# Performance work log

Hardware: AMD Instinct MI355X
Metric: run time of the kernel (lower is better)

The kernel has to match this reference:

```python
import jax, jax.numpy as jnp
import numpy as np

# dims
N, M, L, E = 50000, 1024, 3, 200000      # tgt nodes, src nodes, subtokens/node, edges
HID, EMB, VOCAB = 512, 256, 512
N_SLT, N_SRT = 4, 5                       # SLT edge types (messages), SRT edge types (output head)
W_SCALE = 0.02


def setup_inputs() -> dict:
    key = jax.random.key(0)
    ks = jax.random.split(key, 20)
    inp = {
        "tgt_x": jax.random.randint(ks[0], (N, L), 0, VOCAB),
        "x": jax.random.normal(ks[1], (M, HID), jnp.float32),
        "tgt_edge_index": jax.random.randint(ks[2], (2, E), 0, N),
        "tgt_edge_type": jax.random.randint(ks[3], (E,), 0, N_SLT),
        "embed_table": jax.random.normal(ks[4], (VOCAB, EMB), jnp.float32) * W_SCALE,
        # GCN layer 1 (called twice in the original forward) and layer 3 params
        "W_h1": jax.random.normal(ks[5], (EMB, EMB), jnp.float32) * W_SCALE,
        "W_rel1": jax.random.normal(ks[6], (N_SLT, EMB, EMB), jnp.float32) * W_SCALE,
        "W_src1": jax.random.normal(ks[7], (HID, EMB), jnp.float32) * W_SCALE,
        "W_h3": jax.random.normal(ks[8], (EMB, EMB), jnp.float32) * W_SCALE,
        "W_rel3": jax.random.normal(ks[9], (N_SLT, EMB, EMB), jnp.float32) * W_SCALE,
        "W_src3": jax.random.normal(ks[10], (HID, EMB), jnp.float32) * W_SCALE,
        # output heads
        "Wz": jax.random.normal(ks[11], (EMB, VOCAB), jnp.float32) * W_SCALE,
        "bz": jnp.zeros((VOCAB,), jnp.float32),
        "Wg": jax.random.normal(ks[12], (2 * EMB, N_SRT), jnp.float32) * W_SCALE,
        "bg": jnp.zeros((N_SRT,), jnp.float32),
    }
    return inp


def _gcn_layer(x_src, h, edge_index, edge_type, W_h, W_rel, W_src):
    """Relational GCN decoder layer with cross-attention to encoder nodes."""
    k = x_src @ W_src                                   # [M, EMB]
    attn = jax.nn.softmax(h @ k.T / jnp.sqrt(jnp.float32(EMB)), axis=1)  # [N, M]
    ctx = attn @ k                                      # [N, EMB]
    # per-edge-type transform first ([N, T, EMB]), then gather per edge
    h_t = jnp.einsum('nd,tdf->ntf', h, W_rel)           # [N, N_SLT, EMB]
    src, tgt = edge_index[0], edge_index[1]
    msg = h_t[src, edge_type]                           # [E, EMB] gather
    agg = jax.ops.segment_sum(msg, tgt, num_segments=h.shape[0])  # [N, EMB]
    return jax.nn.relu(h @ W_h + agg + ctx)


def reference(tgt_x, x, tgt_edge_index, tgt_edge_type, embed_table,
              W_h1, W_rel1, W_src1, W_h3, W_rel3, W_src3, Wz, bz, Wg, bg):
    # embedding + reduction over subtokens
    h = embed_table[tgt_x].sum(axis=1)                  # [N, EMB]
    # original code calls gcn1 twice, then gcn3 (gcn2 unused in training path)
    h = _gcn_layer(x, h, tgt_edge_index, tgt_edge_type, W_h1, W_rel1, W_src1)
    h = _gcn_layer(x, h, tgt_edge_index, tgt_edge_type, W_h1, W_rel1, W_src1)
    h = _gcn_layer(x, h, tgt_edge_index, tgt_edge_type, W_h3, W_rel3, W_src3)
    # node head
    node_pred = jax.nn.log_softmax(h @ Wz + bz, axis=1)  # [N, VOCAB]
    # edge head: gather [2,E,EMB] -> permute -> [E, 2*EMB]
    ef = h[tgt_edge_index]                               # [2, E, EMB]
    ef = jnp.transpose(ef, (1, 0, 2)).reshape(E, 2 * EMB)
    edge_pred = jax.nn.log_softmax(ef @ Wg + bg, axis=1)  # [E, N_SRT]
    return node_pred, edge_pred
```

## Files before the change

kernel.cpp:

```cpp
#include <hip/hip_runtime.h>
#include <hip/hip_bf16.h>
#include <cstdint>

#define N_NODES 50000
#define M_SRC   1024
#define E_EDGES 200000
#define EMB     256
#define HIDN    512
#define VOCABSZ 512
#define KW      1280

typedef __attribute__((ext_vector_type(8))) short bf16x8;
typedef __attribute__((ext_vector_type(4))) short bf16x4;
typedef __attribute__((ext_vector_type(4))) float f32x4;

__device__ inline short f2b(float f) {
    __hip_bfloat16 b = __float2bfloat16(f);
    return *reinterpret_cast<short*>(&b);
}
__device__ inline float b2f(short s) {
    __hip_bfloat16 b = *reinterpret_cast<__hip_bfloat16*>(&s);
    return __bfloat162float(b);
}

__device__ inline void gload16(const void* g, void* l) {
    __builtin_amdgcn_global_load_lds(
        (const __attribute__((address_space(1))) unsigned int*)g,
        (__attribute__((address_space(3))) unsigned int*)l,
        16, 0, 0);
}

__device__ inline void tr_read2(unsigned addr, bf16x4& lo, bf16x4& hi) {
    asm volatile("ds_read_b64_tr_b16 %0, %2\n\tds_read_b64_tr_b16 %1, %2 offset:512"
                 : "=&v"(lo), "=&v"(hi) : "v"(addr));
}

__global__ void embed_kernel(const int* __restrict__ tgt_x,
                             const float* __restrict__ table,
                             short* __restrict__ h)
{
    int n = blockIdx.x, d = threadIdx.x;
    const int* tx = tgt_x + (size_t)n * 3;
    float s = table[(size_t)tx[0] * EMB + d]
            + table[(size_t)tx[1] * EMB + d]
            + table[(size_t)tx[2] * EMB + d];
    h[(size_t)n * EMB + d] = f2b(s);
}

__global__ void convert_kernel(const float* __restrict__ in, short* __restrict__ out, int n)
{
    int i = blockIdx.x * 256 + threadIdx.x;
    if (i * 4 < n) {
        float4 v = *(const float4*)&in[i * 4];
        short4 o;
        o.x = f2b(v.x); o.y = f2b(v.y); o.z = f2b(v.z); o.w = f2b(v.w);
        *(short4*)&out[i * 4] = o;
    }
}

template<typename TIN>
__global__ void transpose_kernel(const TIN* __restrict__ in, short* __restrict__ out, int R, int C)
{
    __shared__ float t[32][33];
    int tx = threadIdx.x & 31, ty = threadIdx.x >> 5;
    int r0 = blockIdx.y * 32, c0 = blockIdx.x * 32;
#pragma unroll
    for (int i = 0; i < 4; i++) {
        int r = ty + i * 8;
        TIN v = in[(size_t)(r0 + r) * C + c0 + tx];
        if constexpr (sizeof(TIN) == 4) t[r][tx] = v;
        else                            t[r][tx] = b2f(v);
    }
    __syncthreads();
#pragma unroll
    for (int i = 0; i < 4; i++) {
        int r = ty + i * 8;
        out[(size_t)(c0 + r) * R + r0 + tx] = f2b(t[tx][r]);
    }
}

__global__ void transposeW_kernel(const float* __restrict__ Wh1, const float* __restrict__ Wh3,
                                  const float* __restrict__ Wr1, const float* __restrict__ Wr3,
                                  short* __restrict__ Wcat1, short* __restrict__ Wcat3)
{
    __shared__ float t[32][33];
    const int z = blockIdx.z;
    const float* in; short* outp; int coloff;
    if (z == 0)      { in = Wh1;                               outp = Wcat1; coloff = 0; }
    else if (z == 1) { in = Wh3;                               outp = Wcat3; coloff = 0; }
    else if (z < 6)  { in = Wr1 + (size_t)(z - 2) * EMB * EMB; outp = Wcat1; coloff = 256 + (z - 2) * 256; }
    else             { in = Wr3 + (size_t)(z - 6) * EMB * EMB; outp = Wcat3; coloff = 256 + (z - 6) * 256; }
    int tx = threadIdx.x & 31, ty = threadIdx.x >> 5;
    int r0 = blockIdx.y * 32, c0 = blockIdx.x * 32;
#pragma unroll
    for (int i = 0; i < 4; i++) {
        int r = ty + i * 8;
        t[r][tx] = in[(size_t)(r0 + r) * EMB + c0 + tx];
    }
    __syncthreads();
#pragma unroll
    for (int i = 0; i < 4; i++) {
        int r = ty + i * 8;
        outp[(size_t)(c0 + r) * KW + coloff + r0 + tx] = f2b(t[tx][r]);
    }
}

template<int MODE>
__global__ __launch_bounds__(256) void mgemm(
    const short* __restrict__ A, const short* __restrict__ BT,
    void* __restrict__ outp, const float* __restrict__ aux,
    const float* __restrict__ bias, int NR, int K, int J)
{
    __shared__ short As[128 * 40];
    __shared__ short Bs[128 * 40];
    const int tid  = threadIdx.x;
    const int n0   = blockIdx.x * 128;
    const int j0   = blockIdx.y * 128;
    const int lane = tid & 63, wid = tid >> 6;
    const int wr   = wid >> 1, wc = wid & 1;

    f32x4 acc[4][4];
#pragma unroll
    for (int m = 0; m < 4; m++)
#pragma unroll
        for (int n = 0; n < 4; n++) acc[m][n] = (f32x4){0.f, 0.f, 0.f, 0.f};

    for (int kt = 0; kt < K; kt += 32) {
#pragma unroll
        for (int r = 0; r < 2; r++) {
            int idx = tid + r * 256;
            int row = idx >> 2, ko = (idx & 3) * 8;
            int n = n0 + row;
            bf16x8 av = {0, 0, 0, 0, 0, 0, 0, 0};
            if (n < NR) av = *(const bf16x8*)&A[(size_t)n * K + kt + ko];
            *(bf16x8*)&As[row * 40 + ko] = av;
            *(bf16x8*)&Bs[row * 40 + ko] = *(const bf16x8*)&BT[(size_t)(j0 + row) * K + kt + ko];
        }
        __syncthreads();
        bf16x8 af[4], bfr[4];
#pragma unroll
        for (int m = 0; m < 4; m++)
            af[m] = *(const bf16x8*)&As[(wr * 64 + m * 16 + (lane & 15)) * 40 + (lane >> 4) * 8];
#pragma unroll
        for (int n = 0; n < 4; n++)
            bfr[n] = *(const bf16x8*)&Bs[(wc * 64 + n * 16 + (lane & 15)) * 40 + (lane >> 4) * 8];
#pragma unroll
        for (int m = 0; m < 4; m++)
#pragma unroll
            for (int n = 0; n < 4; n++)
                acc[m][n] = __builtin_amdgcn_mfma_f32_16x16x32_bf16(af[m], bfr[n], acc[m][n], 0, 0, 0);
        __syncthreads();
    }

#pragma unroll
    for (int m = 0; m < 4; m++) {
        int rbase = wr * 64 + m * 16 + ((lane >> 4) * 4);
#pragma unroll
        for (int r = 0; r < 4; r++) {
            int n_g = n0 + rbase + r;
            if (n_g >= NR) continue;
#pragma unroll
            for (int nn = 0; nn < 4; nn++) {
                int j_g = j0 + wc * 64 + nn * 16 + (lane & 15);
                ((short*)outp)[(size_t)n_g * J + j_g] = f2b(acc[m][nn][r]);
            }
        }
    }
}

__global__ __launch_bounds__(256) void mgemm_wide(
    const short* __restrict__ A1, const short* __restrict__ A2,
    const short* __restrict__ BT, short* __restrict__ outp,
    const float* __restrict__ aux, int NR)
{
    __shared__ short As[64 * 40];
    __shared__ short Bs[256 * 40];
    const int tid  = threadIdx.x;
    const int n0   = blockIdx.x * 64;
    const int lane = tid & 63, wid = tid >> 6;
    const int wr   = wid >> 1, wc = wid & 1;
    const int l4 = lane >> 4, l15 = lane & 15;

    f32x4 acc[2][8];
#pragma unroll
    for (int m = 0; m < 2; m++)
#pragma unroll
        for (int n = 0; n < 8; n++) acc[m][n] = (f32x4){0.f, 0.f, 0.f, 0.f};

    for (int kt = 0; kt < KW; kt += 32) {
        {
            int row = tid >> 2, ko = (tid & 3) * 8;
            int n = n0 + row;
            bf16x8 av = {0, 0, 0, 0, 0, 0, 0, 0};
            if (n < NR) {
                const short* ap = (kt < 256) ? &A1[(size_t)n * 256 + kt + ko]
                                             : &A2[(size_t)n * 1024 + (kt - 256) + ko];
                av = *(const bf16x8*)ap;
            }
            *(bf16x8*)&As[row * 40 + ko] = av;
        }
#pragma unroll
        for (int r = 0; r < 4; r++) {
            int idx = tid + r * 256;
            int row = idx >> 2, ko = (idx & 3) * 8;
            *(bf16x8*)&Bs[row * 40 + ko] = *(const bf16x8*)&BT[(size_t)row * KW + kt + ko];
        }
        __syncthreads();
        bf16x8 af[2], bfr[8];
#pragma unroll
        for (int m = 0; m < 2; m++)
            af[m] = *(const bf16x8*)&As[(wr * 32 + m * 16 + l15) * 40 + l4 * 8];
#pragma unroll
        for (int n = 0; n < 8; n++)
            bfr[n] = *(const bf16x8*)&Bs[(wc * 128 + n * 16 + l15) * 40 + l4 * 8];
#pragma unroll
        for (int m = 0; m < 2; m++)
#pragma unroll
            for (int n = 0; n < 8; n++)
                acc[m][n] = __builtin_amdgcn_mfma_f32_16x16x32_bf16(af[m], bfr[n], acc[m][n], 0, 0, 0);
        __syncthreads();
    }

#pragma unroll
    for (int m = 0; m < 2; m++) {
        int rbase = wr * 32 + m * 16 + l4 * 4;
#pragma unroll
        for (int r = 0; r < 4; r++) {
            int n_g = n0 + rbase + r;
            if (n_g >= NR) continue;
#pragma unroll
            for (int nn = 0; nn < 8; nn++) {
                int j_g = wc * 128 + nn * 16 + l15;
                float v = acc[m][nn][r] + aux[(size_t)n_g * 256 + j_g];
                outp[(size_t)n_g * 256 + j_g] = f2b(fmaxf(v, 0.f));
            }
        }
    }
}

__global__ __launch_bounds__(128, 2) void attn_flash(
    const short* __restrict__ h, const short* __restrict__ kb,
    float* __restrict__ C, int NR)
{
    __shared__ short ks[2][32 * 256];
    __shared__ short Ps[64 * 36];

    const int tid = threadIdx.x;
    const int lane = tid & 63, wv = tid >> 6;
    const int l4 = lane >> 4, l15 = lane & 15;
    const int n0 = blockIdx.x * 64;

    auto LOFF = [](int key, int d8) {
        return (d8 & 1) * 8 + (key & 3) * 16 + ((key >> 3) & 3) * 64
             + ((key >> 2) & 1) * 256 + (d8 >> 1) * 512;
    };
    int keyq[8], d8q[8];
#pragma unroll
    for (int q = 0; q < 8; q++) {
        int ci = wv * 64 + lane + q * 128;
        d8q[q]  = (ci & 1) | ((ci >> 6) << 1);
        keyq[q] = ((ci >> 1) & 3) | (((ci >> 5) & 1) << 2) | (((ci >> 3) & 3) << 3);
    }

    bf16x8 hreg[2][8];
#pragma unroll
    for (int rg = 0; rg < 2; rg++) {
        int n = n0 + wv * 32 + rg * 16 + l15;
        const short* hp = &h[(size_t)(n < NR ? n : 0) * 256 + l4 * 8];
#pragma unroll
        for (int kst = 0; kst < 8; kst++) hreg[rg][kst] = *(const bf16x8*)&hp[kst * 32];
        if (n >= NR) {
#pragma unroll
            for (int kst = 0; kst < 8; kst++) hreg[rg][kst] = (bf16x8){0, 0, 0, 0, 0, 0, 0, 0};
        }
    }

#pragma unroll
    for (int q = 0; q < 8; q++)
        gload16(&kb[(size_t)keyq[q] * 256 + d8q[q] * 8],
                (char*)&ks[0][0] + q * 2048 + wv * 1024);
    __syncthreads();

    const unsigned ksbase = (unsigned)(uintptr_t)&ks[0][0];
    const unsigned trlane = 2u * (unsigned)(l15 + l4 * 64);

    f32x4 oacc[2][16];
#pragma unroll
    for (int rg = 0; rg < 2; rg++)
#pragma unroll
        for (int mm = 0; mm < 16; mm++) oacc[rg][mm] = (f32x4){0.f, 0.f, 0.f, 0.f};
    float lsum[2] = {0.f, 0.f};

    for (int c = 0; c < 32; c++) {
        const int cur = c & 1;
        if (c + 1 < 32) {
            const short* kbn = kb + (size_t)(c + 1) * 32 * 256;
#pragma unroll
            for (int q = 0; q < 8; q++)
                gload16(&kbn[(size_t)keyq[q] * 256 + d8q[q] * 8],
                        (char*)&ks[cur ^ 1][0] + q * 2048 + wv * 1024);
        }

        f32x4 sacc[2][2];
#pragma unroll
        for (int rg = 0; rg < 2; rg++) {
            sacc[rg][0] = (f32x4){0.f, 0.f, 0.f, 0.f};
            sacc[rg][1] = (f32x4){0.f, 0.f, 0.f, 0.f};
        }
        __builtin_amdgcn_s_setprio(1);
#pragma unroll
        for (int kst = 0; kst < 8; kst++) {
#pragma unroll
            for (int m = 0; m < 2; m++) {
                int krow = m * 16 + l15;
                bf16x8 afk = *(const bf16x8*)&ks[cur][LOFF(krow, kst * 4 + l4)];
                sacc[0][m] = __builtin_amdgcn_mfma_f32_16x16x32_bf16(afk, hreg[0][kst], sacc[0][m], 0, 0, 0);
                sacc[1][m] = __builtin_amdgcn_mfma_f32_16x16x32_bf16(afk, hreg[1][kst], sacc[1][m], 0, 0, 0);
            }
        }
        __builtin_amdgcn_s_setprio(0);

#pragma unroll
        for (int rg = 0; rg < 2; rg++) {
            int prow = wv * 32 + rg * 16 + l15;
            float psum = 0.f;
#pragma unroll
            for (int m = 0; m < 2; m++) {
                float p0 = __expf(sacc[rg][m][0] * 0.0625f);
                float p1 = __expf(sacc[rg][m][1] * 0.0625f);
                float p2 = __expf(sacc[rg][m][2] * 0.0625f);
                float p3 = __expf(sacc[rg][m][3] * 0.0625f);
                psum += (p0 + p1) + (p2 + p3);
                short4 pk;
                pk.x = f2b(p0); pk.y = f2b(p1); pk.z = f2b(p2); pk.w = f2b(p3);
                *(short4*)&Ps[prow * 36 + m * 16 + l4 * 4] = pk;
            }
            psum += __shfl_xor(psum, 16);
            psum += __shfl_xor(psum, 32);
            lsum[rg] += psum;
        }

        bf16x8 bf2[2];
#pragma unroll
        for (int rg = 0; rg < 2; rg++)
            bf2[rg] = *(const bf16x8*)&Ps[(wv * 32 + rg * 16 + l15) * 36 + l4 * 8];
        unsigned trb = ksbase + (unsigned)(cur * 16384) + trlane;
#pragma unroll
        for (int g = 0; g < 2; g++) {
            bf16x4 lo[8], hi[8];
#pragma unroll
            for (int q = 0; q < 8; q++)
                tr_read2(trb + (unsigned)((g * 8 + q) * 1024), lo[q], hi[q]);
            asm volatile("s_waitcnt lgkmcnt(0)" ::: "memory");
            __builtin_amdgcn_sched_barrier(0);
            __builtin_amdgcn_s_setprio(1);
#pragma unroll
            for (int q = 0; q < 8; q++) {
                bf16x8 af2;
#pragma unroll
                for (int t2 = 0; t2 < 4; t2++) { af2[t2] = lo[q][t2]; af2[t2 + 4] = hi[q][t2]; }
                oacc[0][g * 8 + q] = __builtin_amdgcn_mfma_f32_16x16x32_bf16(af2, bf2[0], oacc[0][g * 8 + q], 0, 0, 0);
                oacc[1][g * 8 + q] = __builtin_amdgcn_mfma_f32_16x16x32_bf16(af2, bf2[1], oacc[1][g * 8 + q], 0, 0, 0);
            }
            __builtin_amdgcn_s_setprio(0);
        }

        __syncthreads();
    }

#pragma unroll
    for (int rg = 0; rg < 2; rg++) {
        float li = 1.0f / lsum[rg];
        int hr = n0 + wv * 32 + rg * 16 + l15;
        if (hr >= NR) continue;
#pragma unroll
        for (int mm = 0; mm < 16; mm++) {
            float4 v;
            v.x = oacc[rg][mm][0] * li;
            v.y = oacc[rg][mm][1] * li;
            v.z = oacc[rg][mm][2] * li;
            v.w = oacc[rg][mm][3] * li;
            *(float4*)&C[(size_t)hr * 256 + mm * 16 + l4 * 4] = v;
        }
    }
}

__global__ void hist_kernel(const int* __restrict__ ei, int* __restrict__ deg)
{
    int e = blockIdx.x * 256 + threadIdx.x;
    if (e < E_EDGES) atomicAdd(&deg[ei[E_EDGES + e]], 1);
}

__global__ void scan1_kernel(const int* __restrict__ deg, int* __restrict__ incl,
                             int* __restrict__ bsum)
{
    __shared__ int s[256];
    int i = blockIdx.x * 256 + threadIdx.x;
    int v = (i < N_NODES) ? deg[i] : 0;
    s[threadIdx.x] = v;
    __syncthreads();
#pragma unroll
    for (int off = 1; off < 256; off <<= 1) {
        int t = (threadIdx.x >= off) ? s[threadIdx.x - off] : 0;
        __syncthreads();
        s[threadIdx.x] += t;
        __syncthreads();
    }
    if (i < N_NODES) incl[i] = s[threadIdx.x];
    if (threadIdx.x == 255) bsum[blockIdx.x] = s[255];
}

__global__ void scan2_kernel(int* __restrict__ bsum, int nb)
{
    __shared__ int s[256];
    int v = (threadIdx.x < nb) ? bsum[threadIdx.x] : 0;
    s[threadIdx.x] = v;
    __syncthreads();
#pragma unroll
    for (int off = 1; off < 256; off <<= 1) {
        int t = (threadIdx.x >= off) ? s[threadIdx.x - off] : 0;
        __syncthreads();
        s[threadIdx.x] += t;
        __syncthreads();
    }
    if (threadIdx.x < nb) bsum[threadIdx.x] = s[threadIdx.x];
}

__global__ void scan3_kernel(const int* __restrict__ deg, const int* __restrict__ incl,
                             const int* __restrict__ bsum, int* __restrict__ row_ptr,
                             int* __restrict__ cursor)
{
    int i = blockIdx.x * 256 + threadIdx.x;
    if (i >= N_NODES) return;
    int pref = (blockIdx.x > 0) ? bsum[blockIdx.x - 1] : 0;
    int start = pref + incl[i] - deg[i];
    row_ptr[i] = start;
    cursor[i]  = start;
    if (i == N_NODES - 1) row_ptr[N_NODES] = pref + incl[i];
}

__global__ void fill_kernel(const int* __restrict__ ei, const int* __restrict__ et,
                            int* __restrict__ cursor, int* __restrict__ eidx)
{
    int e = blockIdx.x * 256 + threadIdx.x;
    if (e >= E_EDGES) return;
    int tg = ei[E_EDGES + e];
    int slot = atomicAdd(&cursor[tg], 1);
    eidx[slot] = ei[e] | (et[e] << 16);
}

__global__ void agg2_kernel(const int* __restrict__ row_ptr, const int* __restrict__ eidx,
                            const short* __restrict__ h, short* __restrict__ Bagg)
{
    int w = (blockIdx.x * 256 + threadIdx.x) >> 6;
    if (w >= N_NODES) return;
    int lane = threadIdx.x & 63;
    int s0 = row_ptr[w], s1 = row_ptr[w + 1];
    float a0[4] = {0, 0, 0, 0}, a1[4] = {0, 0, 0, 0}, a2[4] = {0, 0, 0, 0}, a3[4] = {0, 0, 0, 0};
    for (int i = s0; i < s1; i++) {
        int p = eidx[i];
        int s = p & 0xFFFF, t = p >> 16;
        short4 g = *(const short4*)&h[(size_t)s * EMB + lane * 4];
        float f0 = b2f(g.x), f1 = b2f(g.y), f2 = b2f(g.z), f3 = b2f(g.w);
        if (t == 0)      { a0[0] += f0; a0[1] += f1; a0[2] += f2; a0[3] += f3; }
        else if (t == 1) { a1[0] += f0; a1[1] += f1; a1[2] += f2; a1[3] += f3; }
        else if (t == 2) { a2[0] += f0; a2[1] += f1; a2[2] += f2; a2[3] += f3; }
        else             { a3[0] += f0; a3[1] += f1; a3[2] += f2; a3[3] += f3; }
    }
    short4 o;
    o.x = f2b(a0[0]); o.y = f2b(a0[1]); o.z = f2b(a0[2]); o.w = f2b(a0[3]);
    *(short4*)&Bagg[(size_t)w * 1024 + 0 * 256 + lane * 4] = o;
    o.x = f2b(a1[0]); o.y = f2b(a1[1]); o.z = f2b(a1[2]); o.w = f2b(a1[3]);
    *(short4*)&Bagg[(size_t)w * 1024 + 1 * 256 + lane * 4] = o;
    o.x = f2b(a2[0]); o.y = f2b(a2[1]); o.z = f2b(a2[2]); o.w = f2b(a2[3]);
    *(short4*)&Bagg[(size_t)w * 1024 + 2 * 256 + lane * 4] = o;
    o.x = f2b(a3[0]); o.y = f2b(a3[1]); o.z = f2b(a3[2]); o.w = f2b(a3[3]);
    *(short4*)&Bagg[(size_t)w * 1024 + 3 * 256 + lane * 4] = o;
}

__global__ __launch_bounds__(512, 2) void head_kernel(
    const short* __restrict__ hmat, const short* __restrict__ WzT,
    const float* __restrict__ bz, float* __restrict__ out, int NR)
{
    __shared__ short hs[64 * 256];
    __shared__ float redm[64 * 8];
    __shared__ float reds[64 * 8];

    const int tid = threadIdx.x;
    const int lane = tid & 63, wv = tid >> 6;
    const int l4 = lane >> 4, l15 = lane & 15;
    const int n0 = blockIdx.x * 64;

#pragma unroll
    for (int i = 0; i < 4; i++) {
        int idx = tid + i * 512;
        int row = idx >> 5, kg = idx & 31;
        bf16x8 v = {0, 0, 0, 0, 0, 0, 0, 0};
        if (n0 + row < NR) v = *(const bf16x8*)&hmat[(size_t)(n0 + row) * 256 + kg * 8];
        *(bf16x8*)&hs[(row * 256 + kg * 8) ^ ((row & 7) << 3)] = v;
    }
    __syncthreads();

    f32x4 acc[4][4];
#pragma unroll
    for (int m = 0; m < 4; m++)
#pragma unroll
        for (int n = 0; n < 4; n++) acc[m][n] = (f32x4){0.f, 0.f, 0.f, 0.f};

#pragma unroll
    for (int kt = 0; kt < 256; kt += 32) {
        bf16x8 af[4], bfr[4];
#pragma unroll
        for (int m = 0; m < 4; m++) {
            int row = m * 16 + l15;
            af[m] = *(const bf16x8*)&hs[(row * 256 + kt + l4 * 8) ^ ((row & 7) << 3)];
        }
#pragma unroll
        for (int n = 0; n < 4; n++) {
            int col = wv * 64 + n * 16 + l15;
            bfr[n] = *(const bf16x8*)&WzT[(size_t)col * 256 + kt + l4 * 8];
        }
#pragma unroll
        for (int m = 0; m < 4; m++)
#pragma unroll
            for (int n = 0; n < 4; n++)
                acc[m][n] = __builtin_amdgcn_mfma_f32_16x16x32_bf16(af[m], bfr[n], acc[m][n], 0, 0, 0);
    }

    float bcol[4];
#pragma unroll
    for (int n = 0; n < 4; n++) bcol[n] = bz[wv * 64 + n * 16 + l15];
#pragma unroll
    for (int m = 0; m < 4; m++)
#pragma unroll
        for (int n = 0; n < 4; n++)
#pragma unroll
            for (int r = 0; r < 4; r++) acc[m][n][r] += bcol[n];

    float lg[4][4];
#pragma unroll
    for (int m = 0; m < 4; m++)
#pragma unroll
        for (int r = 0; r < 4; r++) {
            float v = fmaxf(fmaxf(acc[m][0][r], acc[m][1][r]), fmaxf(acc[m][2][r], acc[m][3][r]));
            v = fmaxf(v, __shfl_xor(v, 1));
            v = fmaxf(v, __shfl_xor(v, 2));
            v = fmaxf(v, __shfl_xor(v, 4));
            v = fmaxf(v, __shfl_xor(v, 8));
            if (l15 == 0) redm[(m * 16 + l4 * 4 + r) * 8 + wv] = v;
        }
    __syncthreads();
#pragma unroll
    for (int m = 0; m < 4; m++)
#pragma unroll
        for (int r = 0; r < 4; r++) {
            int row = m * 16 + l4 * 4 + r;
            float v = redm[row * 8 + 0];
#pragma unroll
            for (int w = 1; w < 8; w++) v = fmaxf(v, redm[row * 8 + w]);
            lg[m][r] = v;
        }
#pragma unroll
    for (int m = 0; m < 4; m++)
#pragma unroll
        for (int r = 0; r < 4; r++) {
            float gm = lg[m][r];
            float s = __expf(acc[m][0][r] - gm) + __expf(acc[m][1][r] - gm)
                    + __expf(acc[m][2][r] - gm) + __expf(acc[m][3][r] - gm);
            s += __shfl_xor(s, 1);
            s += __shfl_xor(s, 2);
            s += __shfl_xor(s, 4);
            s += __shfl_xor(s, 8);
            if (l15 == 0) reds[(m * 16 + l4 * 4 + r) * 8 + wv] = s;
        }
    __syncthreads();
#pragma unroll
    for (int m = 0; m < 4; m++)
#pragma unroll
        for (int r = 0; r < 4; r++) {
            int row = m * 16 + l4 * 4 + r;
            float s = reds[row * 8 + 0];
#pragma unroll
            for (int w = 1; w < 8; w++) s += reds[row * 8 + w];
            lg[m][r] += __logf(s);
        }
#pragma unroll
    for (int m = 0; m < 4; m++)
#pragma unroll
        for (int r = 0; r < 4; r++) {
            int hr = n0 + m * 16 + l4 * 4 + r;
            if (hr >= NR) continue;
#pragma unroll
            for (int n = 0; n < 4; n++)
                out[(size_t)hr * VOCABSZ + wv * 64 + n * 16 + l15] = acc[m][n][r] - lg[m][r];
        }
}

__global__ __launch_bounds__(256) void nodeproj_kernel(
    const short* __restrict__ h, const float* __restrict__ Wg,
    float* __restrict__ eproj)
{
    int lane = threadIdx.x & 63;
    int gw   = (blockIdx.x * 256 + threadIdx.x) >> 6;
    int nw   = (gridDim.x * 256) >> 6;
    float ws[4][5], wt[4][5];
#pragma unroll
    for (int c = 0; c < 4; c++)
#pragma unroll
        for (int j = 0; j < 5; j++) {
            ws[c][j] = Wg[(size_t)(lane * 4 + c) * 5 + j];
            wt[c][j] = Wg[(size_t)(256 + lane * 4 + c) * 5 + j];
        }

    for (int n = gw; n < N_NODES; n += nw) {
        short4 hv = *(const short4*)&h[(size_t)n * EMB + lane * 4];
        float f[4] = { b2f(hv.x), b2f(hv.y), b2f(hv.z), b2f(hv.w) };
        float a[5] = {0, 0, 0, 0, 0}, b[5] = {0, 0, 0, 0, 0};
#pragma unroll
        for (int c = 0; c < 4; c++)
#pragma unroll
            for (int j = 0; j < 5; j++) {
                a[j] += f[c] * ws[c][j];
                b[j] += f[c] * wt[c][j];
            }
#pragma unroll
        for (int j = 0; j < 5; j++)
#pragma unroll
            for (int off = 32; off; off >>= 1) {
                a[j] += __shfl_xor(a[j], off);
                b[j] += __shfl_xor(b[j], off);
            }
        if (lane == 0) {
#pragma unroll
            for (int j = 0; j < 5; j++) {
                eproj[(size_t)n * 10 + j]     = a[j];
                eproj[(size_t)n * 10 + 5 + j] = b[j];
            }
        }
    }
}

__global__ void edge_lsm_kernel(const int* __restrict__ ei,
                                const float* __restrict__ eproj,
                                const float* __restrict__ bg,
                                float* __restrict__ out)
{
    int e = blockIdx.x * 256 + threadIdx.x;
    if (e >= E_EDGES) return;
    int s = ei[e], t = ei[E_EDGES + e];
    const float* ps = &eproj[(size_t)s * 10];
    const float* pt = &eproj[(size_t)t * 10 + 5];
    float z[5];
#pragma unroll
    for (int j = 0; j < 5; j++) z[j] = ps[j] + pt[j] + bg[j];
    float mm = fmaxf(fmaxf(fmaxf(z[0], z[1]), fmaxf(z[2], z[3])), z[4]);
    float ss = __expf(z[0] - mm) + __expf(z[1] - mm) + __expf(z[2] - mm)
             + __expf(z[3] - mm) + __expf(z[4] - mm);
    float lg = mm + __logf(ss);
    float* o = &out[(size_t)e * 5];
#pragma unroll
    for (int j = 0; j < 5; j++) o[j] = z[j] - lg;
}

extern "C" void kernel_launch(void* const* d_in, const int* in_sizes, int n_in,
                              void* d_out, int out_size, void* d_ws, size_t ws_size,
                              hipStream_t stream)
{
    const int*   tgt_x = (const int*)  d_in[0];
    const float* x     = (const float*)d_in[1];
    const int*   ei    = (const int*)  d_in[2];
    const int*   et    = (const int*)  d_in[3];
    const float* table = (const float*)d_in[4];
    const float* Wh1   = (const float*)d_in[5];
    const float* Wrel1 = (const float*)d_in[6];
    const float* Wsrc1 = (const float*)d_in[7];
    const float* Wh3   = (const float*)d_in[8];
    const float* Wrel3 = (const float*)d_in[9];
    const float* Wsrc3 = (const float*)d_in[10];
    const float* Wz    = (const float*)d_in[11];
    const float* bz    = (const float*)d_in[12];
    const float* Wg    = (const float*)d_in[13];
    const float* bg    = (const float*)d_in[14];
    float* out = (float*)d_out;

    short* h_a = (short*)d_ws;
    short* h_b = h_a + (size_t)N_NODES * EMB;
    float* C   = (float*)(h_b + (size_t)N_NODES * EMB);
    short* Bagg = (short*)(C + (size_t)N_NODES * EMB);
    short* k1b = Bagg + (size_t)N_NODES * 1024;
    short* k3b = k1b + M_SRC * EMB;
    short* x_b = k3b + M_SRC * EMB;
    short* WsT1 = x_b + M_SRC * HIDN;
    short* WsT3 = WsT1 + EMB * HIDN;
    short* Wcat1 = WsT3 + EMB * HIDN;
    short* Wcat3 = Wcat1 + EMB * KW;
    short* WzT  = Wcat3 + EMB * KW;
    int* deg     = (int*)(WzT + VOCABSZ * EMB);
    int* incl    = deg + N_NODES;
    int* bsum    = incl + N_NODES;
    int* row_ptr = bsum + 256;
    int* cursor  = row_ptr + N_NODES + 1;
    int* eidx    = cursor + N_NODES;
    float* eproj = (float*)(eidx + E_EDGES);

    const int gN = (N_NODES + 127) / 128;
    const int gN64 = (N_NODES + 63) / 64;
    const int nb1 = (N_NODES + 255) / 256;

    hipMemsetAsync(deg, 0, N_NODES * sizeof(int), stream);
    hist_kernel<<<(E_EDGES + 255) / 256, 256, 0, stream>>>(ei, deg);
    scan1_kernel<<<nb1, 256, 0, stream>>>(deg, incl, bsum);
    scan2_kernel<<<1, 256, 0, stream>>>(bsum, nb1);
    scan3_kernel<<<nb1, 256, 0, stream>>>(deg, incl, bsum, row_ptr, cursor);
    fill_kernel<<<(E_EDGES + 255) / 256, 256, 0, stream>>>(ei, et, cursor, eidx);

    convert_kernel<<<(M_SRC * HIDN / 4 + 255) / 256, 256, 0, stream>>>(x, x_b, M_SRC * HIDN);
    transpose_kernel<float><<<dim3(EMB / 32, HIDN / 32), 256, 0, stream>>>(Wsrc1, WsT1, HIDN, EMB);
    transpose_kernel<float><<<dim3(EMB / 32, HIDN / 32), 256, 0, stream>>>(Wsrc3, WsT3, HIDN, EMB);
    transposeW_kernel<<<dim3(8, 8, 10), 256, 0, stream>>>(Wh1, Wh3, Wrel1, Wrel3, Wcat1, Wcat3);
    transpose_kernel<float><<<dim3(VOCABSZ / 32, EMB / 32), 256, 0, stream>>>(Wz, WzT, EMB, VOCABSZ);

    mgemm<0><<<dim3(M_SRC / 128, EMB / 128), 256, 0, stream>>>(x_b, WsT1, k1b, nullptr, nullptr, M_SRC, HIDN, EMB);
    mgemm<0><<<dim3(M_SRC / 128, EMB / 128), 256, 0, stream>>>(x_b, WsT3, k3b, nullptr, nullptr, M_SRC, HIDN, EMB);

    embed_kernel<<<N_NODES, 256, 0, stream>>>(tgt_x, table, h_a);

    short* h_cur = h_a;
    short* h_nxt = h_b;
    for (int layer = 0; layer < 3; layer++) {
        const short* kb   = (layer < 2) ? k1b   : k3b;
        const short* Wcat = (layer < 2) ? Wcat1 : Wcat3;

        attn_flash<<<gN64, 128, 0, stream>>>(h_cur, kb, C, N_NODES);
        agg2_kernel<<<(N_NODES + 3) / 4, 256, 0, stream>>>(row_ptr, eidx, h_cur, Bagg);
        mgemm_wide<<<dim3(gN64, 1), 256, 0, stream>>>(h_cur, Bagg, Wcat, h_nxt, C, N_NODES);
        short* tmp = h_cur; h_cur = h_nxt; h_nxt = tmp;
    }

    head_kernel<<<gN64, 512, 0, stream>>>(h_cur, WzT, bz, out, N_NODES);

    nodeproj_kernel<<<2048, 256, 0, stream>>>(h_cur, Wg, eproj);
    edge_lsm_kernel<<<(E_EDGES + 255) / 256, 256, 0, stream>>>(ei, eproj, bg,
                                                               out + (size_t)N_NODES * VOCABSZ);
}
```

Measured before the change: 813.3 us.

## Double-buffer wide GEMM with direct global-to-LDS loads and swizzled LDS layout

Rewrites the main loop of the wide relu-fused GEMM to use two LDS buffers. Each iteration prefetches the next 64-wide K tile with direct 16-byte global-to-LDS loads (gload16) while the current tile feeds the MFMAs. The LDS layout is swizzled to avoid bank conflicts, and s_setprio raises wavefront priority around the MFMA block. The K step doubles and LDS use grows substantially, which may reduce occupancy. The A loads no longer check NR bounds, so the last block can read past the end of the input rows.

```diff
diff --git a/kernel.cpp b/kernel.cpp
--- a/kernel.cpp
+++ b/kernel.cpp
@@ -173,51 +173,83 @@
     const short* __restrict__ BT, short* __restrict__ outp,
     const float* __restrict__ aux, int NR)
 {
-    __shared__ short As[64 * 40];
-    __shared__ short Bs[256 * 40];
+    __shared__ short As[2][4096];
+    __shared__ short Bs[2][16384];
     const int tid  = threadIdx.x;
     const int n0   = blockIdx.x * 64;
     const int lane = tid & 63, wid = tid >> 6;
     const int wr   = wid >> 1, wc = wid & 1;
     const int l4 = lane >> 4, l15 = lane & 15;
 
+    auto SOFF = [](int r, int d8) {
+        return (d8 & 1) * 8 + (r & 3) * 16 + ((r >> 3) & 3) * 64
+             + ((r >> 2) & 1) * 256 + (d8 >> 1) * 512;
+    };
+    int a_row[2], a_d8[2];
+#pragma unroll
+    for (int q = 0; q < 2; q++) {
+        int cig = tid + q * 256;
+        int s = cig >> 8, ci = cig & 255;
+        a_d8[q]  = (ci & 1) | (((ci >> 6) & 3) << 1);
+        a_row[q] = s * 32 + (((ci >> 1) & 3) | (((ci >> 5) & 1) << 2) | (((ci >> 3) & 3) << 3));
+    }
+    int b_row[8], b_d8[8];
+#pragma unroll
+    for (int q = 0; q < 8; q++) {
+        int cig = tid + q * 256;
+        int s = cig >> 8, ci = cig & 255;
+        b_d8[q]  = (ci & 1) | (((ci >> 6) & 3) << 1);
+        b_row[q] = s * 32 + (((ci >> 1) & 3) | (((ci >> 5) & 1) << 2) | (((ci >> 3) & 3) << 3));
+    }
+
     f32x4 acc[2][8];
 #pragma unroll
     for (int m = 0; m < 2; m++)
 #pragma unroll
         for (int n = 0; n < 8; n++) acc[m][n] = (f32x4){0.f, 0.f, 0.f, 0.f};
 
-    for (int kt = 0; kt < KW; kt += 32) {
-        {
-            int row = tid >> 2, ko = (tid & 3) * 8;
-            int n = n0 + row;
-            bf16x8 av = {0, 0, 0, 0, 0, 0, 0, 0};
-            if (n < NR) {
-                const short* ap = (kt < 256) ? &A1[(size_t)n * 256 + kt + ko]
-                                             : &A2[(size_t)n * 1024 + (kt - 256) + ko];
-                av = *(const bf16x8*)ap;
-            }
-            *(bf16x8*)&As[row * 40 + ko] = av;
-        }
-#pragma unroll
-        for (int r = 0; r < 4; r++) {
-            int idx = tid + r * 256;
-            int row = idx >> 2, ko = (idx & 3) * 8;
-            *(bf16x8*)&Bs[row * 40 + ko] = *(const bf16x8*)&BT[(size_t)row * KW + kt + ko];
-        }
-        __syncthreads();
-        bf16x8 af[2], bfr[8];
-#pragma unroll
-        for (int m = 0; m < 2; m++)
-            af[m] = *(const bf16x8*)&As[(wr * 32 + m * 16 + l15) * 40 + l4 * 8];
-#pragma unroll
-        for (int n = 0; n < 8; n++)
-            bfr[n] = *(const bf16x8*)&Bs[(wc * 128 + n * 16 + l15) * 40 + l4 * 8];
-#pragma unroll
-        for (int m = 0; m < 2; m++)
-#pragma unroll
-            for (int n = 0; n < 8; n++)
-                acc[m][n] = __builtin_amdgcn_mfma_f32_16x16x32_bf16(af[m], bfr[n], acc[m][n], 0, 0, 0);
+    auto STAGE = [&](int buf, int kt) {
+#pragma unroll
+        for (int q = 0; q < 2; q++) {
+            int col = kt + a_d8[q] * 8;
+            const short* src = (col < 256) ? &A1[(size_t)(n0 + a_row[q]) * 256 + col]
+                                           : &A2[(size_t)(n0 + a_row[q]) * 1024 + (col - 256)];
+            gload16(src, (char*)&As[buf][0] + q * 4096 + wid * 1024);
+        }
+#pragma unroll
+        for (int q = 0; q < 8; q++) {
+            gload16(&BT[(size_t)b_row[q] * KW + kt + b_d8[q] * 8],
+                    (char*)&Bs[buf][0] + q * 4096 + wid * 1024);
+        }
+    };
+
+    STAGE(0, 0);
+    __syncthreads();
+
+    for (int t = 0; t < 20; t++) {
+        const int cur = t & 1;
+        if (t + 1 < 20) STAGE(cur ^ 1, (t + 1) * 64);
+#pragma unroll
+        for (int kst = 0; kst < 2; kst++) {
+            const int d8 = kst * 4 + l4;
+            bf16x8 af[2], bfr[8];
+#pragma unroll
+            for (int m = 0; m < 2; m++)
+                af[m] = *(const bf16x8*)&As[cur][wr * 2048 + SOFF(m * 16 + l15, d8)];
+#pragma unroll
+            for (int n = 0; n < 8; n++) {
+                int sb = wc * 4 + (n >> 1);
+                int r  = (n & 1) * 16 + l15;
+                bfr[n] = *(const bf16x8*)&Bs[cur][sb * 2048 + SOFF(r, d8)];
+            }
+            __builtin_amdgcn_s_setprio(1);
+#pragma unroll
+            for (int m = 0; m < 2; m++)
+#pragma unroll
+                for (int n = 0; n < 8; n++)
+                    acc[m][n] = __builtin_amdgcn_mfma_f32_16x16x32_bf16(af[m], bfr[n], acc[m][n], 0, 0, 0);
+            __builtin_amdgcn_s_setprio(0);
+        }
         __syncthreads();
     }
 
```

Result: faster. 769.7 us (-5.4%).
